# Performance work log

Measured on AMD Instinct MI355X. Metric: run time of the kernel, lower is better.

The kernel has to match this reference:

```python
import jax, jax.numpy as jnp
import numpy as np


def setup_inputs() -> dict:
    key = jax.random.key(0)
    kx, kq, kk, kv = jax.random.split(key, 4)
    B, S, D_IN, H, D_OUT = 2, 2048, 768, 12, 64
    scale = 0.02
    return {
        "x": jax.random.normal(kx, (B, S, D_IN), dtype=jnp.float32),
        "Wq": jax.random.normal(kq, (H, D_IN, D_OUT), dtype=jnp.float32) * scale,
        "Wk": jax.random.normal(kk, (H, D_IN, D_OUT), dtype=jnp.float32) * scale,
        "Wv": jax.random.normal(kv, (H, D_IN, D_OUT), dtype=jnp.float32) * scale,
    }


def reference(x, Wq, Wk, Wv):
    # x: [B, S, d_in]; Wq/Wk/Wv: [H, d_in, d_out] (stacked per-head Linear weights, no bias)
    B, S, _ = x.shape
    H, _, d_out = Wq.shape
    q = jnp.einsum("bsd,hde->bhse", x, Wq)  # [B, H, S, d_out]
    k = jnp.einsum("bsd,hde->bhse", x, Wk)
    v = jnp.einsum("bsd,hde->bhse", x, Wv)
    scores = jnp.einsum("bhse,bhte->bhst", q, k) / jnp.sqrt(jnp.float32(d_out))
    causal = jnp.tril(jnp.ones((S, S), dtype=bool))  # True = keep
    scores = jnp.where(causal, scores, jnp.float32(-jnp.inf))
    attn = jax.nn.softmax(scores, axis=-1)  # dropout = 0.0 -> identity
    ctx = jnp.einsum("bhst,bhte->bhse", attn, v)  # [B, H, S, d_out]
    # concat heads along last dim: [B, S, H*d_out]
    return ctx.transpose(0, 2, 1, 3).reshape(B, S, H * d_out)
```

## Files before the change

kernel.cpp:

```cpp
#include <hip/hip_runtime.h>
#include <hip/hip_bf16.h>


typedef short bf16x8 __attribute__((ext_vector_type(8)));
typedef short bf16x4 __attribute__((ext_vector_type(4)));
typedef float f32x4  __attribute__((ext_vector_type(4)));

#define MFMA16(a, b, c)  __builtin_amdgcn_mfma_f32_16x16x32_bf16((a), (b), (c), 0, 0, 0)
#define MFMAK16(a, b, c) __builtin_amdgcn_mfma_f32_16x16x16bf16_1k((a), (b), (c), 0, 0, 0)

static __device__ __forceinline__ unsigned short f2bf(float f) {
    unsigned int u = __builtin_bit_cast(unsigned int, f);
    u += 0x7fffu + ((u >> 16) & 1u);
    return (unsigned short)(u >> 16);
}

static __device__ __forceinline__ int sw(int row, int cb) {
    return (row << 7) + (cb ^ ((row & 7) << 4));
}

static __device__ __forceinline__ void gld16(const void* g, void* l) {
    __builtin_amdgcn_global_load_lds(
        (__attribute__((address_space(1))) void*)g,
        (__attribute__((address_space(3))) void*)l, 16, 0, 0);
}

__global__ __launch_bounds__(256) void prep(const float* __restrict__ x,
                                            const float* __restrict__ Wq,
                                            const float* __restrict__ Wk,
                                            const float* __restrict__ Wv,
                                            char* __restrict__ xb,
                                            char* __restrict__ wtb) {
    __shared__ float tile[64][65];
    const int bid = blockIdx.x;
    const int t = threadIdx.x;
    if (bid < 768) {
        const int stile = bid & 63, ks = bid >> 6;
        const int row = t >> 2, k16 = (t & 3) * 16;
        const float* src = x + (size_t)(stile * 64 + row) * 768 + ks * 64 + k16;
        char* img = xb + ((size_t)stile * 12 + ks) * 8192;
        const float4 v0 = *(const float4*)(src);
        const float4 v1 = *(const float4*)(src + 4);
        const float4 v2 = *(const float4*)(src + 8);
        const float4 v3 = *(const float4*)(src + 12);
        bf16x8 o0, o1;
        o0[0] = (short)f2bf(v0.x); o0[1] = (short)f2bf(v0.y);
        o0[2] = (short)f2bf(v0.z); o0[3] = (short)f2bf(v0.w);
        o0[4] = (short)f2bf(v1.x); o0[5] = (short)f2bf(v1.y);
        o0[6] = (short)f2bf(v1.z); o0[7] = (short)f2bf(v1.w);
        o1[0] = (short)f2bf(v2.x); o1[1] = (short)f2bf(v2.y);
        o1[2] = (short)f2bf(v2.z); o1[3] = (short)f2bf(v2.w);
        o1[4] = (short)f2bf(v3.x); o1[5] = (short)f2bf(v3.y);
        o1[6] = (short)f2bf(v3.z); o1[7] = (short)f2bf(v3.w);
        *(bf16x8*)(img + sw(row, k16 * 2)) = o0;
        *(bf16x8*)(img + sw(row, k16 * 2 + 16)) = o1;
    } else {
        const int idx = bid - 768;
        const int wh = idx % 36, dt = idx / 36;
        const int w = wh / 12, h = wh % 12;
        const float* W = (w == 0) ? Wq : (w == 1) ? Wk : Wv;
        for (int i = 0; i < 4; ++i) {
            int c = t + i * 256;
            int d = c >> 4, e4 = (c & 15) * 4;
            const float4 v = *(const float4*)(W + (size_t)(h * 768 + dt * 64 + d) * 64 + e4);
            tile[d][e4 + 0] = v.x; tile[d][e4 + 1] = v.y;
            tile[d][e4 + 2] = v.z; tile[d][e4 + 3] = v.w;
        }
        __syncthreads();
        char* img = wtb + ((size_t)(wh * 12) + dt) * 8192;
        for (int i = 0; i < 4; ++i) {
            int c = t + i * 256;
            int e = c >> 4, d4 = (c & 15) * 4;
            ushort4 o;
            o.x = f2bf(tile[d4 + 0][e]); o.y = f2bf(tile[d4 + 1][e]);
            o.z = f2bf(tile[d4 + 2][e]); o.w = f2bf(tile[d4 + 3][e]);
            *(ushort4*)(img + e * 128 + ((d4 * 2) ^ ((e & 7) << 4))) = o;
        }
    }
}

__global__ __launch_bounds__(256) void proj_qkv(const char* __restrict__ xb,
                                                const char* __restrict__ wtb,
                                                unsigned short* __restrict__ q,
                                                unsigned short* __restrict__ ksw,
                                                char* __restrict__ vsw) {
    __shared__ __align__(16) char smem[65536];
    const int stile = blockIdx.x;
    const int h = blockIdx.y;
    const int t = threadIdx.x;
    const int wave = t >> 6, lane = t & 63;
    const int lhi = lane >> 4, llo = lane & 15;
    const int wr = wave >> 1, wc = wave & 1;

    const char* asrc = xb + (size_t)stile * 12 * 8192;

    f32x4 acc[3][2][2] = {};

    #define STAGE(KS, BUF)                                                       \
        do {                                                                     \
            const char* s0 = asrc + (KS) * 8192;                                 \
            char* d0 = smem + (BUF) * 32768;                                     \
            gld16(s0 + t * 16, d0 + t * 16);                                     \
            gld16(s0 + t * 16 + 4096, d0 + t * 16 + 4096);                       \
            for (int w3 = 0; w3 < 3; ++w3) {                                     \
                const char* s1 = wtb + ((size_t)((w3 * 12 + h) * 12) + (KS)) * 8192; \
                char* d1 = smem + (BUF) * 32768 + (1 + w3) * 8192;               \
                gld16(s1 + t * 16, d1 + t * 16);                                 \
                gld16(s1 + t * 16 + 4096, d1 + t * 16 + 4096);                   \
            }                                                                    \
        } while (0)

    STAGE(0, 0);
    __syncthreads();
    int cur = 0;
    for (int ks = 0; ks < 12; ++ks) {
        if (ks < 11) STAGE(ks + 1, cur ^ 1);
        char* Alds = smem + cur * 32768;
        #pragma unroll
        for (int kk = 0; kk < 2; ++kk) {
            bf16x8 a[2];
            #pragma unroll
            for (int m = 0; m < 2; ++m)
                a[m] = *(const bf16x8*)(Alds + sw(wr * 32 + m * 16 + llo, kk * 64 + lhi * 16));
            #pragma unroll
            for (int w3 = 0; w3 < 3; ++w3) {
                char* Blds = Alds + (1 + w3) * 8192;
                #pragma unroll
                for (int n = 0; n < 2; ++n) {
                    bf16x8 b = *(const bf16x8*)(Blds + sw(wc * 32 + n * 16 + llo, kk * 64 + lhi * 16));
                    #pragma unroll
                    for (int m = 0; m < 2; ++m)
                        acc[w3][m][n] = MFMA16(a[m], b, acc[w3][m][n]);
                }
            }
        }
        __syncthreads();
        cur ^= 1;
    }
    #undef STAGE

    const float SCALE_Q = 0.18033688011112042f;
    const int bglob = stile >> 5, ktile = stile & 31;
    const int bh = bglob * 12 + h;
    #pragma unroll
    for (int m = 0; m < 2; ++m)
        for (int n = 0; n < 2; ++n)
            for (int r = 0; r < 4; ++r) {
                int s = (stile * 64 + wr * 32 + m * 16 + lhi * 4 + r) & 2047;
                int e = wc * 32 + n * 16 + llo;
                q[(size_t)(bh * 2048 + s) * 64 + e] = f2bf(acc[0][m][n][r] * SCALE_Q);
            }
    unsigned short* kdst = ksw + ((size_t)bh * 32 + ktile) * 4096;
    #pragma unroll
    for (int m = 0; m < 2; ++m)
        for (int n = 0; n < 2; ++n)
            for (int r = 0; r < 4; ++r) {
                int kk = wr * 32 + m * 16 + lhi * 4 + r;
                int e = wc * 32 + n * 16 + llo;
                kdst[kk * 64 + (e ^ ((kk & 7) << 3))] = f2bf(acc[1][m][n][r]);
            }
    char* vtimg = smem;
    __syncthreads();
    #pragma unroll
    for (int m = 0; m < 2; ++m)
        for (int n = 0; n < 2; ++n)
            for (int r = 0; r < 4; ++r) {
                int kk = wr * 32 + m * 16 + lhi * 4 + r;
                int e = wc * 32 + n * 16 + llo;
                int pos = (((kk >> 2) & 3) * 32 + (kk >> 4) * 8 + (kk & 3) * 2) ^ ((e & 7) << 4);
                *(unsigned short*)(vtimg + e * 128 + pos) = f2bf(acc[2][m][n][r]);
            }
    __syncthreads();
    {
        char* dst = vsw + ((size_t)bh * 32 + ktile) * 8192;
        #pragma unroll
        for (int i = 0; i < 2; ++i)
            *(float4*)(dst + t * 16 + i * 4096) =
                *(const float4*)(vtimg + t * 16 + i * 4096);
    }
}

__global__ __launch_bounds__(256) void attn(const unsigned short* __restrict__ Q,
                                            const char* __restrict__ Ksw,
                                            const char* __restrict__ Vsw,
                                            float* __restrict__ out) {
    __shared__ __align__(16) char smem[32768];
    const int t = threadIdx.x, wave = t >> 6, lane = t & 63;
    const int lhi = lane >> 4, llo = lane & 15;
    const int bid = blockIdx.x;
    const int tt = bid & 31, grp = (bid >> 5) & 7, e3 = bid >> 8;
    const int qt = (e3 == 0) ? tt
                 : (e3 == 1) ? ((tt + 16) & 31)
                             : ((tt < 16) ? 30 - 2 * tt : 63 - 2 * tt);
    const int bh = grp * 3 + e3;
    const unsigned short* Qg = Q + (size_t)bh * 2048 * 64;
    const char* Kg = Ksw + (size_t)bh * 32 * 8192;
    const char* Vg = Vsw + (size_t)bh * 32 * 8192;

    const int q0 = qt * 64 + wave * 16;
    bf16x8 qa[2];
    #pragma unroll
    for (int kk = 0; kk < 2; ++kk)
        qa[kk] = *(const bf16x8*)(Qg + (size_t)(q0 + llo) * 64 + kk * 32 + lhi * 8);

    f32x4 acc[4] = {};
    float m_r = -1e30f, l_r = 0.f;

    #define ASTAGE(KT, BUF)                                              \
        do {                                                             \
            const char* ks_ = Kg + (size_t)(KT) * 8192;                  \
            const char* vs_ = Vg + (size_t)(KT) * 8192;                  \
            char* kd = smem + (BUF) * 8192;                              \
            char* vd = smem + 16384 + (BUF) * 8192;                      \
            gld16(ks_ + t * 16, kd + t * 16);                            \
            gld16(ks_ + t * 16 + 4096, kd + t * 16 + 4096);              \
            gld16(vs_ + t * 16, vd + t * 16);                            \
            gld16(vs_ + t * 16 + 4096, vd + t * 16 + 4096);              \
        } while (0)

    ASTAGE(0, 0);
    __syncthreads();
    int cur = 0;
    for (int kt = 0; kt <= qt; ++kt) {
        if (kt < qt) ASTAGE(kt + 1, cur ^ 1);
        char* Kb = smem + cur * 8192;
        char* Vb = smem + 16384 + cur * 8192;

        f32x4 sc[4];
        __builtin_amdgcn_s_setprio(1);
        #pragma unroll
        for (int n = 0; n < 4; ++n) {
            f32x4 z = {};
            #pragma unroll
            for (int kk = 0; kk < 2; ++kk) {
                bf16x8 bk = *(const bf16x8*)(Kb + sw(n * 16 + llo, kk * 64 + lhi * 16));
                z = MFMA16(bk, qa[kk], z);
            }
            sc[n] = z;
        }
        __builtin_amdgcn_s_setprio(0);
        if (kt == qt) {
            #pragma unroll
            for (int n = 0; n < 4; ++n)
                #pragma unroll
                for (int r = 0; r < 4; ++r)
                    if (kt * 64 + n * 16 + lhi * 4 + r > q0 + llo) sc[n][r] = -1e30f;
        }
        float pmax = fmaxf(
            fmaxf(fmaxf(fmaxf(sc[0][0], sc[0][1]), fmaxf(sc[0][2], sc[0][3])),
                  fmaxf(fmaxf(sc[1][0], sc[1][1]), fmaxf(sc[1][2], sc[1][3]))),
            fmaxf(fmaxf(fmaxf(sc[2][0], sc[2][1]), fmaxf(sc[2][2], sc[2][3])),
                  fmaxf(fmaxf(sc[3][0], sc[3][1]), fmaxf(sc[3][2], sc[3][3]))));
        if (__any(pmax > m_r + 8.0f)) {
            float tm = fmaxf(pmax, __shfl_xor(pmax, 16, 64));
            tm = fmaxf(tm, __shfl_xor(tm, 32, 64));
            float nm = fmaxf(m_r, tm);
            float corr = exp2f(m_r - nm);
            m_r = nm;
            l_r *= corr;
            #pragma unroll
            for (int n = 0; n < 4; ++n)
                #pragma unroll
                for (int r = 0; r < 4; ++r) acc[n][r] *= corr;
        }
        bf16x4 pf[4];
        float ps = 0.f;
        #pragma unroll
        for (int kb = 0; kb < 4; ++kb) {
            float p0 = exp2f(sc[kb][0] - m_r), p1 = exp2f(sc[kb][1] - m_r);
            float p2 = exp2f(sc[kb][2] - m_r), p3 = exp2f(sc[kb][3] - m_r);
            ps += (p0 + p1) + (p2 + p3);
            unsigned int w0, w1;
            asm("v_cvt_pk_bf16_f32 %0, %1, %2" : "=v"(w0) : "v"(p0), "v"(p1));
            asm("v_cvt_pk_bf16_f32 %0, %1, %2" : "=v"(w1) : "v"(p2), "v"(p3));
            unsigned long long u = ((unsigned long long)w1 << 32) | w0;
            pf[kb] = __builtin_bit_cast(bf16x4, u);
        }
        l_r += ps;
        __builtin_amdgcn_s_setprio(1);
        #pragma unroll
        for (int n = 0; n < 4; ++n) {
            const int row = n * 16 + llo;
            bf16x8 v8a = *(const bf16x8*)(Vb + sw(row, lhi * 32));
            bf16x8 v8b = *(const bf16x8*)(Vb + sw(row, lhi * 32 + 16));
            f32x4 a = acc[n];
            a = MFMAK16(__builtin_shufflevector(v8a, v8a, 0, 1, 2, 3), pf[0], a);
            a = MFMAK16(__builtin_shufflevector(v8a, v8a, 4, 5, 6, 7), pf[1], a);
            a = MFMAK16(__builtin_shufflevector(v8b, v8b, 0, 1, 2, 3), pf[2], a);
            a = MFMAK16(__builtin_shufflevector(v8b, v8b, 4, 5, 6, 7), pf[3], a);
            acc[n] = a;
        }
        __builtin_amdgcn_s_setprio(0);
        __syncthreads();
        cur ^= 1;
    }
    #undef ASTAGE
    l_r += __shfl_xor(l_r, 16, 64);
    l_r += __shfl_xor(l_r, 32, 64);
    const float inv = 1.0f / l_r;
    const int b = bh / 12, h = bh - b * 12;
    #pragma unroll
    for (int n = 0; n < 4; ++n) {
        float4 o;
        o.x = acc[n][0] * inv; o.y = acc[n][1] * inv;
        o.z = acc[n][2] * inv; o.w = acc[n][3] * inv;
        *(float4*)(out + (size_t)(b * 2048 + q0 + llo) * 768 + h * 64 + n * 16 + lhi * 4) = o;
    }
}

extern "C" void kernel_launch(void* const* d_in, const int* in_sizes, int n_in,
                              void* d_out, int out_size, void* d_ws, size_t ws_size,
                              hipStream_t stream) {
    const float* x  = (const float*)d_in[0];
    const float* Wq = (const float*)d_in[1];
    const float* Wk = (const float*)d_in[2];
    const float* Wv = (const float*)d_in[3];
    float* out = (float*)d_out;

    char* ws = (char*)d_ws;
    char*           wtb = ws;
    unsigned short* q   = (unsigned short*)(ws + 3538944);
    unsigned short* ksw = (unsigned short*)(ws + 9830400);
    char*           vsw = (char*)(ws + 16121856);
    char*           xb  = (char*)(ws + 22413312);

    hipLaunchKernelGGL(prep, dim3(1200), dim3(256), 0, stream, x, Wq, Wk, Wv, xb, wtb);
    hipLaunchKernelGGL(proj_qkv, dim3(64, 12), dim3(256), 0, stream,
                       xb, wtb, q, ksw, vsw);
    hipLaunchKernelGGL(attn, dim3(768), dim3(256), 0, stream, q, (const char*)ksw, vsw, out);
}
```

Measured before the change: 71.08 us.

## Process 128-row query tiles per block with two row groups per wave

Each attention block now covers 128 query rows instead of 64, and each wave handles two 16-row groups. Every K/V tile staged in LDS is therefore reused by twice as many queries, which roughly halves K/V global and LDS traffic per query, and the grid shrinks from 768 to 384 blocks. Block order is remapped so the longest causal tiles are scheduled first, with the short tiles filling in afterwards for load balance. In exchange, register pressure rises (two accumulator sets), waves in the upper half idle on the final diagonal tile, and 384 blocks may under-fill the 256 CUs in a second wave.

```diff
diff --git a/kernel.cpp b/kernel.cpp
--- a/kernel.cpp
+++ b/kernel.cpp
@@ -188,23 +188,31 @@
     const int t = threadIdx.x, wave = t >> 6, lane = t & 63;
     const int lhi = lane >> 4, llo = lane & 15;
     const int bid = blockIdx.x;
-    const int tt = bid & 31, grp = (bid >> 5) & 7, e3 = bid >> 8;
-    const int qt = (e3 == 0) ? tt
-                 : (e3 == 1) ? ((tt + 16) & 31)
-                             : ((tt < 16) ? 30 - 2 * tt : 63 - 2 * tt);
-    const int bh = grp * 3 + e3;
+    int pt, bh;
+    if (bid < 256) {
+        pt = 15 - bid / 24; bh = bid % 24;
+    } else {
+        int i = bid - 256;
+        if (i < 120) { pt = i / 24; bh = i % 24; }
+        else         { pt = 5; bh = 16 + (i - 120); }
+    }
     const unsigned short* Qg = Q + (size_t)bh * 2048 * 64;
     const char* Kg = Ksw + (size_t)bh * 32 * 8192;
     const char* Vg = Vsw + (size_t)bh * 32 * 8192;
 
-    const int q0 = qt * 64 + wave * 16;
-    bf16x8 qa[2];
-    #pragma unroll
-    for (int kk = 0; kk < 2; ++kk)
-        qa[kk] = *(const bf16x8*)(Qg + (size_t)(q0 + llo) * 64 + kk * 32 + lhi * 8);
-
-    f32x4 acc[4] = {};
-    float m_r = -1e30f, l_r = 0.f;
+    const int q0w = pt * 128 + wave * 32;
+    const int ktmax_w = 2 * pt + (wave >> 1);
+    const int ktlast = 2 * pt + 1;
+
+    bf16x8 qa[2][2];
+    #pragma unroll
+    for (int g = 0; g < 2; ++g)
+        #pragma unroll
+        for (int kk = 0; kk < 2; ++kk)
+            qa[g][kk] = *(const bf16x8*)(Qg + (size_t)(q0w + g * 16 + llo) * 64 + kk * 32 + lhi * 8);
+
+    f32x4 acc[2][4] = {};
+    float m_r[2] = {-1e30f, -1e30f}, l_r[2] = {0.f, 0.f};
 
     #define ASTAGE(KT, BUF)                                              \
         do {                                                             \
@@ -221,90 +229,115 @@
     ASTAGE(0, 0);
     __syncthreads();
     int cur = 0;
-    for (int kt = 0; kt <= qt; ++kt) {
-        if (kt < qt) ASTAGE(kt + 1, cur ^ 1);
-        char* Kb = smem + cur * 8192;
-        char* Vb = smem + 16384 + cur * 8192;
-
-        f32x4 sc[4];
-        __builtin_amdgcn_s_setprio(1);
+    for (int kt = 0; kt <= ktlast; ++kt) {
+        if (kt < ktlast) ASTAGE(kt + 1, cur ^ 1);
+        if (kt <= ktmax_w) {
+            char* Kb = smem + cur * 8192;
+            char* Vb = smem + 16384 + cur * 8192;
+
+            f32x4 sc[2][4] = {};
+            __builtin_amdgcn_s_setprio(1);
+            #pragma unroll
+            for (int n = 0; n < 4; ++n) {
+                #pragma unroll
+                for (int kk = 0; kk < 2; ++kk) {
+                    bf16x8 bk = *(const bf16x8*)(Kb + sw(n * 16 + llo, kk * 64 + lhi * 16));
+                    sc[0][n] = MFMA16(bk, qa[0][kk], sc[0][n]);
+                    sc[1][n] = MFMA16(bk, qa[1][kk], sc[1][n]);
+                }
+            }
+            __builtin_amdgcn_s_setprio(0);
+            if (kt == ktmax_w) {
+                #pragma unroll
+                for (int g = 0; g < 2; ++g)
+                    #pragma unroll
+                    for (int n = 0; n < 4; ++n)
+                        #pragma unroll
+                        for (int r = 0; r < 4; ++r)
+                            if (kt * 64 + n * 16 + lhi * 4 + r > q0w + g * 16 + llo)
+                                sc[g][n][r] = -1e30f;
+            }
+            float pmax[2];
+            #pragma unroll
+            for (int g = 0; g < 2; ++g)
+                pmax[g] = fmaxf(
+                    fmaxf(fmaxf(fmaxf(sc[g][0][0], sc[g][0][1]), fmaxf(sc[g][0][2], sc[g][0][3])),
+                          fmaxf(fmaxf(sc[g][1][0], sc[g][1][1]), fmaxf(sc[g][1][2], sc[g][1][3]))),
+                    fmaxf(fmaxf(fmaxf(sc[g][2][0], sc[g][2][1]), fmaxf(sc[g][2][2], sc[g][2][3])),
+                          fmaxf(fmaxf(sc[g][3][0], sc[g][3][1]), fmaxf(sc[g][3][2], sc[g][3][3]))));
+            if (__any(pmax[0] > m_r[0] + 8.0f || pmax[1] > m_r[1] + 8.0f)) {
+                #pragma unroll
+                for (int g = 0; g < 2; ++g) {
+                    float tm = fmaxf(pmax[g], __shfl_xor(pmax[g], 16, 64));
+                    tm = fmaxf(tm, __shfl_xor(tm, 32, 64));
+                    float nm = fmaxf(m_r[g], tm);
+                    float corr = exp2f(m_r[g] - nm);
+                    m_r[g] = nm;
+                    l_r[g] *= corr;
+                    #pragma unroll
+                    for (int n = 0; n < 4; ++n)
+                        #pragma unroll
+                        for (int r = 0; r < 4; ++r) acc[g][n][r] *= corr;
+                }
+            }
+            bf16x4 pf[2][4];
+            #pragma unroll
+            for (int g = 0; g < 2; ++g) {
+                float ps = 0.f;
+                #pragma unroll
+                for (int kb = 0; kb < 4; ++kb) {
+                    float p0 = exp2f(sc[g][kb][0] - m_r[g]), p1 = exp2f(sc[g][kb][1] - m_r[g]);
+                    float p2 = exp2f(sc[g][kb][2] - m_r[g]), p3 = exp2f(sc[g][kb][3] - m_r[g]);
+                    ps += (p0 + p1) + (p2 + p3);
+                    unsigned int w0, w1;
+                    asm("v_cvt_pk_bf16_f32 %0, %1, %2" : "=v"(w0) : "v"(p0), "v"(p1));
+                    asm("v_cvt_pk_bf16_f32 %0, %1, %2" : "=v"(w1) : "v"(p2), "v"(p3));
+                    unsigned long long u = ((unsigned long long)w1 << 32) | w0;
+                    pf[g][kb] = __builtin_bit_cast(bf16x4, u);
+                }
+                l_r[g] += ps;
+            }
+            __builtin_amdgcn_s_setprio(1);
+            #pragma unroll
+            for (int n = 0; n < 4; ++n) {
+                const int row = n * 16 + llo;
+                bf16x8 v8a = *(const bf16x8*)(Vb + sw(row, lhi * 32));
+                bf16x8 v8b = *(const bf16x8*)(Vb + sw(row, lhi * 32 + 16));
+                bf16x4 vf0 = __builtin_shufflevector(v8a, v8a, 0, 1, 2, 3);
+                bf16x4 vf1 = __builtin_shufflevector(v8a, v8a, 4, 5, 6, 7);
+                bf16x4 vf2 = __builtin_shufflevector(v8b, v8b, 0, 1, 2, 3);
+                bf16x4 vf3 = __builtin_shufflevector(v8b, v8b, 4, 5, 6, 7);
+                #pragma unroll
+                for (int g = 0; g < 2; ++g) {
+                    f32x4 a = acc[g][n];
+                    a = MFMAK16(vf0, pf[g][0], a);
+                    a = MFMAK16(vf1, pf[g][1], a);
+                    a = MFMAK16(vf2, pf[g][2], a);
+                    a = MFMAK16(vf3, pf[g][3], a);
+                    acc[g][n] = a;
+                }
+            }
+            __builtin_amdgcn_s_setprio(0);
+        }
+        __syncthreads();
+        cur ^= 1;
+    }
+    #undef ASTAGE
+    const int b = bh / 12, h = bh - b * 12;
+    #pragma unroll
+    for (int g = 0; g < 2; ++g) {
+        float lr = l_r[g];
+        lr += __shfl_xor(lr, 16, 64);
+        lr += __shfl_xor(lr, 32, 64);
+        const float inv = 1.0f / lr;
+        const int qrow = q0w + g * 16 + llo;
         #pragma unroll
         for (int n = 0; n < 4; ++n) {
-            f32x4 z = {};
-            #pragma unroll
-            for (int kk = 0; kk < 2; ++kk) {
-                bf16x8 bk = *(const bf16x8*)(Kb + sw(n * 16 + llo, kk * 64 + lhi * 16));
-                z = MFMA16(bk, qa[kk], z);
-            }
-            sc[n] = z;
-        }
-        __builtin_amdgcn_s_setprio(0);
-        if (kt == qt) {
-            #pragma unroll
-            for (int n = 0; n < 4; ++n)
-                #pragma unroll
-                for (int r = 0; r < 4; ++r)
-                    if (kt * 64 + n * 16 + lhi * 4 + r > q0 + llo) sc[n][r] = -1e30f;
-        }
-        float pmax = fmaxf(
-            fmaxf(fmaxf(fmaxf(sc[0][0], sc[0][1]), fmaxf(sc[0][2], sc[0][3])),
-                  fmaxf(fmaxf(sc[1][0], sc[1][1]), fmaxf(sc[1][2], sc[1][3]))),
-            fmaxf(fmaxf(fmaxf(sc[2][0], sc[2][1]), fmaxf(sc[2][2], sc[2][3])),
-                  fmaxf(fmaxf(sc[3][0], sc[3][1]), fmaxf(sc[3][2], sc[3][3]))));
-        if (__any(pmax > m_r + 8.0f)) {
-            float tm = fmaxf(pmax, __shfl_xor(pmax, 16, 64));
-            tm = fmaxf(tm, __shfl_xor(tm, 32, 64));
-            float nm = fmaxf(m_r, tm);
-            float corr = exp2f(m_r - nm);
-            m_r = nm;
-            l_r *= corr;
-            #pragma unroll
-            for (int n = 0; n < 4; ++n)
-                #pragma unroll
-                for (int r = 0; r < 4; ++r) acc[n][r] *= corr;
-        }
-        bf16x4 pf[4];
-        float ps = 0.f;
-        #pragma unroll
-        for (int kb = 0; kb < 4; ++kb) {
-            float p0 = exp2f(sc[kb][0] - m_r), p1 = exp2f(sc[kb][1] - m_r);
-            float p2 = exp2f(sc[kb][2] - m_r), p3 = exp2f(sc[kb][3] - m_r);
-            ps += (p0 + p1) + (p2 + p3);
-            unsigned int w0, w1;
-            asm("v_cvt_pk_bf16_f32 %0, %1, %2" : "=v"(w0) : "v"(p0), "v"(p1));
-            asm("v_cvt_pk_bf16_f32 %0, %1, %2" : "=v"(w1) : "v"(p2), "v"(p3));
-            unsigned long long u = ((unsigned long long)w1 << 32) | w0;
-            pf[kb] = __builtin_bit_cast(bf16x4, u);
-        }
-        l_r += ps;
-        __builtin_amdgcn_s_setprio(1);
-        #pragma unroll
-        for (int n = 0; n < 4; ++n) {
-            const int row = n * 16 + llo;
-            bf16x8 v8a = *(const bf16x8*)(Vb + sw(row, lhi * 32));
-            bf16x8 v8b = *(const bf16x8*)(Vb + sw(row, lhi * 32 + 16));
-            f32x4 a = acc[n];
-            a = MFMAK16(__builtin_shufflevector(v8a, v8a, 0, 1, 2, 3), pf[0], a);
-            a = MFMAK16(__builtin_shufflevector(v8a, v8a, 4, 5, 6, 7), pf[1], a);
-            a = MFMAK16(__builtin_shufflevector(v8b, v8b, 0, 1, 2, 3), pf[2], a);
-            a = MFMAK16(__builtin_shufflevector(v8b, v8b, 4, 5, 6, 7), pf[3], a);
-            acc[n] = a;
-        }
-        __builtin_amdgcn_s_setprio(0);
-        __syncthreads();
-        cur ^= 1;
-    }
-    #undef ASTAGE
-    l_r += __shfl_xor(l_r, 16, 64);
-    l_r += __shfl_xor(l_r, 32, 64);
-    const float inv = 1.0f / l_r;
-    const int b = bh / 12, h = bh - b * 12;
-    #pragma unroll
-    for (int n = 0; n < 4; ++n) {
-        float4 o;
-        o.x = acc[n][0] * inv; o.y = acc[n][1] * inv;
-        o.z = acc[n][2] * inv; o.w = acc[n][3] * inv;
-        *(float4*)(out + (size_t)(b * 2048 + q0 + llo) * 768 + h * 64 + n * 16 + lhi * 4) = o;
+            float4 o;
+            o.x = acc[g][n][0] * inv; o.y = acc[g][n][1] * inv;
+            o.z = acc[g][n][2] * inv; o.w = acc[g][n][3] * inv;
+            *(float4*)(out + (size_t)(b * 2048 + qrow) * 768 + h * 64 + n * 16 + lhi * 4) = o;
+        }
     }
 }
 
@@ -327,5 +360,5 @@
     hipLaunchKernelGGL(prep, dim3(1200), dim3(256), 0, stream, x, Wq, Wk, Wv, xb, wtb);
     hipLaunchKernelGGL(proj_qkv, dim3(64, 12), dim3(256), 0, stream,
                        xb, wtb, q, ksw, vsw);
-    hipLaunchKernelGGL(attn, dim3(768), dim3(256), 0, stream, q, (const char*)ksw, vsw, out);
-}
+    hipLaunchKernelGGL(attn, dim3(384), dim3(256), 0, stream, q, (const char*)ksw, vsw, out);
+}
```

Result: slower. 83.45 us (+17.4%).
